# Performance work log

Hardware: AMD Instinct MI355X
Metric: run time of the kernel (lower is better)

## Reference

```python
import jax, jax.numpy as jnp
import numpy as np

B, T, N = 512, 512, 128   # batch, timesteps, driving series
M = 64                    # LSTM hidden size
UNITS = 64                # attention units


def setup_inputs() -> dict:
    key = jax.random.key(0)
    ks = jax.random.split(key, 9)
    s = lambda fan_in: 1.0 / np.sqrt(fan_in)
    return {
        "x": jax.random.normal(ks[0], (B, T, N), jnp.float32),
        "hidden_state": jax.random.normal(ks[1], (B, M), jnp.float32),
        "cell_state": jax.random.normal(ks[2], (B, M), jnp.float32),
        # Dense(units) applied to x permuted to (B, N, T): kernel contracts T
        "w1_kernel": jax.random.normal(ks[3], (T, UNITS), jnp.float32) * s(T),
        "w1_bias": jnp.zeros((UNITS,), jnp.float32),
        # Dense(units) applied to query (B, N, 2M)
        "w2_kernel": jax.random.normal(ks[4], (2 * M, UNITS), jnp.float32) * s(2 * M),
        "w2_bias": jnp.zeros((UNITS,), jnp.float32),
        # Dense(1) scoring
        "v_kernel": jax.random.normal(ks[5], (UNITS, 1), jnp.float32) * s(UNITS),
        "v_bias": jnp.zeros((1,), jnp.float32),
    }


def reference(x, hidden_state, cell_state, w1_kernel, w1_bias,
              w2_kernel, w2_bias, v_kernel, v_bias):
    # query: (B, 2M) -> broadcast over the N feature axis (RepeatVector)
    query = jnp.concatenate([hidden_state, cell_state], axis=-1)
    q_proj = query @ w2_kernel + w2_bias                    # (B, UNITS)
    x_perm = jnp.transpose(x, (0, 2, 1))                    # (B, N, T)
    score = jnp.tanh(x_perm @ w1_kernel + w1_bias + q_proj[:, None, :])  # (B, N, UNITS)
    score = score @ v_kernel + v_bias                       # (B, N, 1)
    score = jnp.transpose(score, (0, 2, 1))                 # (B, 1, N)
    attention_weights = jax.nn.softmax(score, axis=-1)      # (B, 1, N)
    context_vector = jnp.sum(attention_weights * x, axis=-1)  # (B, T)
    return context_vector, attention_weights
```

## Files before the change

### kernel.cpp

```cpp
#include <hip/hip_runtime.h>
#include <hip/hip_bf16.h>

namespace {

constexpr int kB = 512, kT = 512, kN = 128, kM = 64, kU = 64;
constexpr int TT = 64;

__device__ __forceinline__ float fast_tanh(float x) {
  return 1.0f - 2.0f / (__expf(2.0f * x) + 1.0f);
}

struct Smem {
  float xs[TT][kN];
  float w1s[TT][kU];
  float qp[kU];
  float sred[16][kN + 1];
  float sn[kN];
  float aw[kN];
};

__global__ __launch_bounds__(256) void fused_kernel(
    const float* __restrict__ x,
    const float* __restrict__ hs,
    const float* __restrict__ cs,
    const float* __restrict__ w1,
    const float* __restrict__ w1b,
    const float* __restrict__ w2,
    const float* __restrict__ w2b,
    const float* __restrict__ vk,
    const float* __restrict__ vb,
    float* __restrict__ ctx_out,
    float* __restrict__ aw_out)
{
  __shared__ Smem s;
  const int b = blockIdx.x;
  const int tid = threadIdx.x;

  if (tid < kU) {
    float a0 = w2b[tid] + w1b[tid];
    for (int k = 0; k < kM; ++k)
      a0 = fmaf(hs[(size_t)b * kM + k], w2[k * kU + tid], a0);
    for (int k = 0; k < kM; ++k)
      a0 = fmaf(cs[(size_t)b * kM + k], w2[(kM + k) * kU + tid], a0);
    s.qp[tid] = a0;
  }

  const int n0 = (tid >> 4) * 8;
  const int u0 = (tid & 15) * 4;

  float acc[8][4];
#pragma unroll
  for (int j = 0; j < 8; ++j)
#pragma unroll
    for (int i = 0; i < 4; ++i) acc[j][i] = 0.f;

  for (int t0 = 0; t0 < kT; t0 += TT) {
    __syncthreads();
    {
      const float4* xp = (const float4*)(x + ((size_t)b * kT + t0) * kN);
#pragma unroll
      for (int i = 0; i < 8; ++i) {
        int idx = tid + i * 256;
        *(float4*)&s.xs[idx >> 5][(idx & 31) * 4] = xp[idx];
      }
      const float4* wp = (const float4*)(w1 + (size_t)t0 * kU);
#pragma unroll
      for (int i = 0; i < 4; ++i) {
        int idx = tid + i * 256;
        *(float4*)&s.w1s[idx >> 4][(idx & 15) * 4] = wp[idx];
      }
    }
    __syncthreads();

#pragma unroll 4
    for (int tt = 0; tt < TT; ++tt) {
      float xv[8], wv[4];
      *(float4*)&xv[0] = *(const float4*)&s.xs[tt][n0];
      *(float4*)&xv[4] = *(const float4*)&s.xs[tt][n0 + 4];
      *(float4*)&wv[0] = *(const float4*)&s.w1s[tt][u0];
#pragma unroll
      for (int j = 0; j < 8; ++j)
#pragma unroll
        for (int i = 0; i < 4; ++i)
          acc[j][i] = fmaf(xv[j], wv[i], acc[j][i]);
    }
  }

  float qv[4], vv[4];
#pragma unroll
  for (int i = 0; i < 4; ++i) {
    qv[i] = s.qp[u0 + i];
    vv[i] = vk[u0 + i];
  }
#pragma unroll
  for (int j = 0; j < 8; ++j) {
    float p = 0.f;
#pragma unroll
    for (int i = 0; i < 4; ++i)
      p = fmaf(fast_tanh(acc[j][i] + qv[i]), vv[i], p);
    s.sred[tid & 15][n0 + j] = p;
  }
  __syncthreads();
  if (tid < kN) {
    float v = vb[0];
#pragma unroll
    for (int g = 0; g < 16; ++g) v += s.sred[g][tid];
    s.sn[tid] = v;
  }
  __syncthreads();

  if (tid < 64) {
    float s0 = s.sn[tid], s1 = s.sn[tid + 64];
    float m = fmaxf(s0, s1);
#pragma unroll
    for (int off = 32; off > 0; off >>= 1) m = fmaxf(m, __shfl_xor(m, off));
    float e0 = __expf(s0 - m), e1 = __expf(s1 - m);
    float se = e0 + e1;
#pragma unroll
    for (int off = 32; off > 0; off >>= 1) se += __shfl_xor(se, off);
    float inv = 1.0f / se;
    float a0 = e0 * inv, a1 = e1 * inv;
    s.aw[tid] = a0;
    s.aw[tid + 64] = a1;
    aw_out[(size_t)b * kN + tid] = a0;
    aw_out[(size_t)b * kN + tid + 64] = a1;
  }
  __syncthreads();

  const int lr = tid & 3;
  const int qrow = tid >> 2;
  for (int rg = 0; rg < 8; ++rg) {
    const int r = rg * 64 + qrow;
    const float4* xp = (const float4*)(x + ((size_t)b * kT + r) * kN);
    float a = 0.f;
#pragma unroll
    for (int k = 0; k < 8; ++k) {
      int i = lr + k * 4;
      float4 v = xp[i];
      const float* w = &s.aw[i * 4];
      a = fmaf(v.x, w[0], a);
      a = fmaf(v.y, w[1], a);
      a = fmaf(v.z, w[2], a);
      a = fmaf(v.w, w[3], a);
    }
    a += __shfl_xor(a, 1);
    a += __shfl_xor(a, 2);
    if (lr == 0) ctx_out[(size_t)b * kT + r] = a;
  }
}

}

extern "C" void kernel_launch(void* const* d_in, const int* in_sizes, int n_in,
                              void* d_out, int out_size, void* d_ws, size_t ws_size,
                              hipStream_t stream) {
  const float* x   = (const float*)d_in[0];
  const float* hs  = (const float*)d_in[1];
  const float* cs  = (const float*)d_in[2];
  const float* w1  = (const float*)d_in[3];
  const float* w1b = (const float*)d_in[4];
  const float* w2  = (const float*)d_in[5];
  const float* w2b = (const float*)d_in[6];
  const float* vk  = (const float*)d_in[7];
  const float* vb  = (const float*)d_in[8];

  float* out = (float*)d_out;
  float* ctx = out;
  float* awo = out + (size_t)kB * kT;

  hipLaunchKernelGGL(fused_kernel, dim3(kB), dim3(256), 0, stream,
                     x, hs, cs, w1, w1b, w2, w2b, vk, vb, ctx, awo);
}
```

Baseline: 248.2 us.

## Compute x·W1 projection with split-bf16 MFMA instead of FP32 FMAs

Replaces the per-thread FP32 outer-product loop with bf16 MFMA 16x16x32 instructions. Each FP32 value is split into hi and lo bf16 halves, and three MFMAs (hi*hi, hi*lo, lo*hi) approximate FP32 accuracy. x and W1 tiles are stored transposed in LDS as packed hi/lo words with padding. Blocks grow to 512 threads, and the score reduction moves from a shared-memory array to wavefront shuffles. The scalar v bias is dropped because softmax is shift-invariant. The cost is extra packing work during loads and a small precision loss.

```diff
diff --git a/kernel.cpp b/kernel.cpp
--- a/kernel.cpp
+++ b/kernel.cpp
@@ -5,21 +5,46 @@
 
 constexpr int kB = 512, kT = 512, kN = 128, kM = 64, kU = 64;
 constexpr int TT = 64;
+constexpr int SX = 68;
+
+typedef __attribute__((ext_vector_type(8))) short short8;
+typedef __attribute__((ext_vector_type(4))) float f32x4;
+
+__device__ __forceinline__ unsigned pack_hl(float v) {
+  unsigned u = __float_as_uint(v);
+  unsigned hs = (u + 0x7fffu + ((u >> 16) & 1u)) >> 16;
+  float lo = v - __uint_as_float(hs << 16);
+  unsigned ul = __float_as_uint(lo);
+  unsigned ls = (ul + 0x7fffu + ((ul >> 16) & 1u)) >> 16;
+  return (hs << 16) | (ls & 0xffffu);
+}
 
 __device__ __forceinline__ float fast_tanh(float x) {
   return 1.0f - 2.0f / (__expf(2.0f * x) + 1.0f);
 }
 
+union FragU { unsigned u[4]; short8 s; };
+
+__device__ __forceinline__ void unpack_hl(const unsigned* p, short8& hi, short8& lo) {
+  FragU H, L;
+#pragma unroll
+  for (int j = 0; j < 4; ++j) {
+    unsigned a = p[2 * j], b = p[2 * j + 1];
+    H.u[j] = (a >> 16) | (b & 0xffff0000u);
+    L.u[j] = (a & 0xffffu) | (b << 16);
+  }
+  hi = H.s; lo = L.s;
+}
+
 struct Smem {
-  float xs[TT][kN];
-  float w1s[TT][kU];
+  unsigned xsT[kN * SX];
+  unsigned w1T[kU * SX];
   float qp[kU];
-  float sred[16][kN + 1];
   float sn[kN];
   float aw[kN];
 };
 
-__global__ __launch_bounds__(256) void fused_kernel(
+__global__ __launch_bounds__(512, 4) void fused_kernel(
     const float* __restrict__ x,
     const float* __restrict__ hs,
     const float* __restrict__ cs,
@@ -45,67 +70,96 @@
     s.qp[tid] = a0;
   }
 
-  const int n0 = (tid >> 4) * 8;
-  const int u0 = (tid & 15) * 4;
-
-  float acc[8][4];
-#pragma unroll
-  for (int j = 0; j < 8; ++j)
-#pragma unroll
-    for (int i = 0; i < 4; ++i) acc[j][i] = 0.f;
+  const int lane = tid & 63;
+  const int w8 = tid >> 6;
+  const int c = lane & 15;
+  const int q = lane >> 4;
+
+  f32x4 acc[4];
+#pragma unroll
+  for (int ut = 0; ut < 4; ++ut) acc[ut] = (f32x4){0.f, 0.f, 0.f, 0.f};
+
+  const int n2 = tid & 63;
+  const int halfx = tid >> 6;
+  const int u2 = tid & 31;
+  const int grpw = tid >> 5;
 
   for (int t0 = 0; t0 < kT; t0 += TT) {
     __syncthreads();
+#pragma unroll
+    for (int qi = 0; qi < 2; ++qi) {
+      const int tq = halfx + 8 * qi;
+      unsigned p0[4], p1[4];
+#pragma unroll
+      for (int j = 0; j < 4; ++j) {
+        float2 v = *(const float2*)&x[((size_t)b * kT + t0 + 4 * tq + j) * kN + 2 * n2];
+        p0[j] = pack_hl(v.x);
+        p1[j] = pack_hl(v.y);
+      }
+      *(uint4*)&s.xsT[(2 * n2) * SX + 4 * tq]     = make_uint4(p0[0], p0[1], p0[2], p0[3]);
+      *(uint4*)&s.xsT[(2 * n2 + 1) * SX + 4 * tq] = make_uint4(p1[0], p1[1], p1[2], p1[3]);
+    }
     {
-      const float4* xp = (const float4*)(x + ((size_t)b * kT + t0) * kN);
-#pragma unroll
-      for (int i = 0; i < 8; ++i) {
-        int idx = tid + i * 256;
-        *(float4*)&s.xs[idx >> 5][(idx & 31) * 4] = xp[idx];
-      }
-      const float4* wp = (const float4*)(w1 + (size_t)t0 * kU);
-#pragma unroll
-      for (int i = 0; i < 4; ++i) {
-        int idx = tid + i * 256;
-        *(float4*)&s.w1s[idx >> 4][(idx & 15) * 4] = wp[idx];
-      }
+      const int tq = grpw;
+      unsigned p0[4], p1[4];
+#pragma unroll
+      for (int j = 0; j < 4; ++j) {
+        float2 v = *(const float2*)&w1[(size_t)(t0 + 4 * tq + j) * kU + 2 * u2];
+        p0[j] = pack_hl(v.x);
+        p1[j] = pack_hl(v.y);
+      }
+      *(uint4*)&s.w1T[(2 * u2) * SX + 4 * tq]     = make_uint4(p0[0], p0[1], p0[2], p0[3]);
+      *(uint4*)&s.w1T[(2 * u2 + 1) * SX + 4 * tq] = make_uint4(p1[0], p1[1], p1[2], p1[3]);
     }
     __syncthreads();
 
-#pragma unroll 4
-    for (int tt = 0; tt < TT; ++tt) {
-      float xv[8], wv[4];
-      *(float4*)&xv[0] = *(const float4*)&s.xs[tt][n0];
-      *(float4*)&xv[4] = *(const float4*)&s.xs[tt][n0 + 4];
-      *(float4*)&wv[0] = *(const float4*)&s.w1s[tt][u0];
-#pragma unroll
-      for (int j = 0; j < 8; ++j)
-#pragma unroll
-        for (int i = 0; i < 4; ++i)
-          acc[j][i] = fmaf(xv[j], wv[i], acc[j][i]);
+#pragma unroll
+    for (int kk = 0; kk < TT; kk += 32) {
+      short8 ahi, alo;
+      {
+        unsigned raw[8];
+        const unsigned* pa = &s.xsT[(16 * w8 + c) * SX + kk + 8 * q];
+        *(uint4*)&raw[0] = *(const uint4*)pa;
+        *(uint4*)&raw[4] = *(const uint4*)(pa + 4);
+        unpack_hl(raw, ahi, alo);
+      }
+#pragma unroll
+      for (int ut = 0; ut < 4; ++ut) {
+        unsigned raw[8];
+        const unsigned* pb = &s.w1T[(16 * ut + c) * SX + kk + 8 * q];
+        *(uint4*)&raw[0] = *(const uint4*)pb;
+        *(uint4*)&raw[4] = *(const uint4*)(pb + 4);
+        short8 bhi, blo;
+        unpack_hl(raw, bhi, blo);
+        acc[ut] = __builtin_amdgcn_mfma_f32_16x16x32_bf16(ahi, bhi, acc[ut], 0, 0, 0);
+        acc[ut] = __builtin_amdgcn_mfma_f32_16x16x32_bf16(ahi, blo, acc[ut], 0, 0, 0);
+        acc[ut] = __builtin_amdgcn_mfma_f32_16x16x32_bf16(alo, bhi, acc[ut], 0, 0, 0);
+      }
     }
   }
 
   float qv[4], vv[4];
 #pragma unroll
-  for (int i = 0; i < 4; ++i) {
-    qv[i] = s.qp[u0 + i];
-    vv[i] = vk[u0 + i];
-  }
-#pragma unroll
-  for (int j = 0; j < 8; ++j) {
+  for (int ut = 0; ut < 4; ++ut) {
+    qv[ut] = s.qp[16 * ut + c];
+    vv[ut] = vk[16 * ut + c];
+  }
+  float pr[4];
+#pragma unroll
+  for (int r = 0; r < 4; ++r) {
     float p = 0.f;
 #pragma unroll
-    for (int i = 0; i < 4; ++i)
-      p = fmaf(fast_tanh(acc[j][i] + qv[i]), vv[i], p);
-    s.sred[tid & 15][n0 + j] = p;
-  }
-  __syncthreads();
-  if (tid < kN) {
-    float v = vb[0];
-#pragma unroll
-    for (int g = 0; g < 16; ++g) v += s.sred[g][tid];
-    s.sn[tid] = v;
+    for (int ut = 0; ut < 4; ++ut)
+      p = fmaf(fast_tanh(acc[ut][r] + qv[ut]), vv[ut], p);
+    p += __shfl_xor(p, 1);
+    p += __shfl_xor(p, 2);
+    p += __shfl_xor(p, 4);
+    p += __shfl_xor(p, 8);
+    pr[r] = p;
+  }
+  if (c == 0) {
+#pragma unroll
+    for (int r = 0; r < 4; ++r) s.sn[16 * w8 + 4 * q + r] = pr[r];
   }
   __syncthreads();
 
@@ -128,25 +182,27 @@
   __syncthreads();
 
   const int lr = tid & 3;
-  const int qrow = tid >> 2;
-  for (int rg = 0; rg < 8; ++rg) {
-    const int r = rg * 64 + qrow;
+  const int rr = tid >> 2;
+#pragma unroll
+  for (int rg = 0; rg < 4; ++rg) {
+    const int r = rg * 128 + rr;
     const float4* xp = (const float4*)(x + ((size_t)b * kT + r) * kN);
     float a = 0.f;
 #pragma unroll
     for (int k = 0; k < 8; ++k) {
       int i = lr + k * 4;
       float4 v = xp[i];
-      const float* w = &s.aw[i * 4];
-      a = fmaf(v.x, w[0], a);
-      a = fmaf(v.y, w[1], a);
-      a = fmaf(v.z, w[2], a);
-      a = fmaf(v.w, w[3], a);
+      const float* wa = &s.aw[i * 4];
+      a = fmaf(v.x, wa[0], a);
+      a = fmaf(v.y, wa[1], a);
+      a = fmaf(v.z, wa[2], a);
+      a = fmaf(v.w, wa[3], a);
     }
     a += __shfl_xor(a, 1);
     a += __shfl_xor(a, 2);
     if (lr == 0) ctx_out[(size_t)b * kT + r] = a;
   }
+  (void)vb;
 }
 
 }
@@ -168,6 +224,6 @@
   float* ctx = out;
   float* awo = out + (size_t)kB * kT;
 
-  hipLaunchKernelGGL(fused_kernel, dim3(kB), dim3(256), 0, stream,
+  hipLaunchKernelGGL(fused_kernel, dim3(kB), dim3(512), 0, stream,
                      x, hs, cs, w1, w1b, w2, w2b, vk, vb, ctx, awo);
 }
```

After: 226.8 us. -8.6%, faster.
